# Kernel optimization log

Hardware: AMD Instinct MI355X
Metric: run time of the kernel (lower is better)

## Reference

```python
import jax, jax.numpy as jnp
import numpy as np

ID, IH, IW = 8, 16, 16
HEADS, DIM_HEAD = 8, 32
INP, OUP = 256, 256
B = 4
N = ID * IH * IW  # 2048
INNER = HEADS * DIM_HEAD  # 256
SCALE = DIM_HEAD ** -0.5


def _make_relative_pos():
    # Faithful to the torch ctor: 3D coords, pairwise diffs, linearize, shift to >=0
    z, y, x = np.meshgrid(np.arange(ID), np.arange(IH), np.arange(IW), indexing='ij')
    coords = np.stack([z.ravel(), y.ravel(), x.ravel()], axis=1)  # [N,3]
    rel = coords[:, None, :] - coords[None, :, :]                 # [N,N,3]
    rp = rel[:, :, 0] * (IH * IW) + rel[:, :, 1] * IW + rel[:, :, 2]
    rp = rp - rp.min()
    return jnp.asarray(rp, dtype=jnp.int32)                       # [N,N]


def setup_inputs() -> dict:
    key = jax.random.key(0)
    k1, k2, k3, k4, k5 = jax.random.split(key, 5)
    table_size = ID * IH * IW * 8  # 16384, as in nn.Embedding ctor
    return {
        "x": jax.random.normal(k1, (B, N, INP), dtype=jnp.float32),
        "w_qkv": jax.random.normal(k2, (INP, 3 * INNER), dtype=jnp.float32) * (INP ** -0.5),
        "bias_table": jax.random.normal(k3, (table_size, 1), dtype=jnp.float32),
        "w_out": jax.random.normal(k4, (INNER, OUP), dtype=jnp.float32) * (INNER ** -0.5),
        "b_out": jax.random.normal(k5, (OUP,), dtype=jnp.float32),
        "relative_pos": _make_relative_pos(),
    }


def reference(x, w_qkv, bias_table, w_out, b_out, relative_pos):
    Bb, Nn, C = x.shape
    qkv = x @ w_qkv                                   # [B, N, 3*H*D]
    qkv = qkv.reshape(Bb, Nn, 3, HEADS, DIM_HEAD)
    qkv = jnp.transpose(qkv, (2, 0, 3, 1, 4))         # [3, B, H, N, D]
    q, k, v = qkv[0], qkv[1], qkv[2]
    q = q * SCALE
    attn = jnp.einsum('bhnd,bhmd->bhnm', q, k)        # [B, H, N, N]
    bias = bias_table[relative_pos, 0]                # [N, N], shared across B,H
    attn = attn + bias
    attn = jax.nn.softmax(attn, axis=-1)
    out = jnp.einsum('bhnm,bhmd->bhnd', attn, v)      # [B, H, N, D]
    out = jnp.transpose(out, (0, 2, 1, 3)).reshape(Bb, Nn, INNER)
    return out @ w_out + b_out                        # dropout p=0 -> identity
```

## Files before the change

kernel.cpp:

```cpp
#include <hip/hip_runtime.h>

typedef unsigned short u16;
typedef unsigned int u32;
typedef __attribute__((ext_vector_type(8))) short bf16x8;
typedef __attribute__((ext_vector_type(4))) float f32x4;

#define MFMA16(a, b, c) __builtin_amdgcn_mfma_f32_16x16x32_bf16(a, b, c, 0, 0, 0)

__device__ __forceinline__ float hw_exp2(float x) { return __builtin_amdgcn_exp2f(x); }

__device__ __forceinline__ u16 f2bf(float f) {
    union { float f; u32 i; } v; v.f = f;
    u32 x = v.i;
    return (u16)((x + 0x7FFFu + ((x >> 16) & 1u)) >> 16);
}

__global__ __launch_bounds__(256) void k_prep(const float* __restrict__ x,
                                              const float* __restrict__ wqkv,
                                              const float* __restrict__ wout,
                                              u16* __restrict__ xb,
                                              u16* __restrict__ wqkvT,
                                              u16* __restrict__ woutT) {
    const float QSCALE2 = 0.2550566756538019f;
    int bx = blockIdx.x, tid = threadIdx.x;
    if (bx < 1024) {
        int base = bx * 2048 + tid * 8;
        float4 a = *(const float4*)(x + base);
        float4 b = *(const float4*)(x + base + 4);
        uint4 r;
        r.x = f2bf(a.x) | ((u32)f2bf(a.y) << 16);
        r.y = f2bf(a.z) | ((u32)f2bf(a.w) << 16);
        r.z = f2bf(b.x) | ((u32)f2bf(b.y) << 16);
        r.w = f2bf(b.z) | ((u32)f2bf(b.w) << 16);
        *(uint4*)(xb + base) = r;
    } else if (bx < 1792) {
        int idx = (bx - 1024) * 256 + tid;
        int n = idx >> 8, kk = idx & 255;
        float sc = (n < 256) ? QSCALE2 : 1.0f;
        wqkvT[idx] = f2bf(wqkv[kk * 768 + n] * sc);
    } else {
        int idx = (bx - 1792) * 256 + tid;
        int n = idx >> 8, kk = idx & 255;
        woutT[idx] = f2bf(wout[kk * 256 + n]);
    }
}

__global__ __launch_bounds__(256) void k_gemm_qkv(const u16* __restrict__ xb,
                                                  const u16* __restrict__ wT,
                                                  u16* __restrict__ qkv) {
    __shared__ __align__(16) u16 slds[8704];
    const int tid = threadIdx.x;
    const int wave = tid >> 6, lane = tid & 63, quad = lane >> 4, ql = lane & 15;
    const int mbase = blockIdx.x * 128 + (wave & 1) * 64;
    const int nbase = blockIdx.y * 64 + (wave >> 1) * 32;
    f32x4 acc[4][2];
#pragma unroll
    for (int i = 0; i < 4; ++i)
#pragma unroll
        for (int j = 0; j < 2; ++j) acc[i][j] = (f32x4){0.f, 0.f, 0.f, 0.f};
#pragma unroll
    for (int ks = 0; ks < 8; ++ks) {
        bf16x8 af[4], bfm[2];
#pragma unroll
        for (int ms = 0; ms < 4; ++ms)
            af[ms] = *(const bf16x8*)(xb + (size_t)(mbase + ms * 16 + ql) * 256 + ks * 32 + quad * 8);
#pragma unroll
        for (int ns = 0; ns < 2; ++ns)
            bfm[ns] = *(const bf16x8*)(wT + (size_t)(nbase + ns * 16 + ql) * 256 + ks * 32 + quad * 8);
#pragma unroll
        for (int ms = 0; ms < 4; ++ms)
#pragma unroll
            for (int ns = 0; ns < 2; ++ns)
                acc[ms][ns] = MFMA16(af[ms], bfm[ns], acc[ms][ns]);
    }

    const int t = (blockIdx.y * 64) >> 8;
    if (t < 2) {
        const int rowb = (wave & 1) * 64, colb = (wave >> 1) * 32;
#pragma unroll
        for (int ms = 0; ms < 4; ++ms)
#pragma unroll
            for (int ns = 0; ns < 2; ++ns)
#pragma unroll
                for (int r = 0; r < 4; ++r)
                    slds[(rowb + ms * 16 + quad * 4 + r) * 68 + colb + ns * 16 + ql] =
                        f2bf(acc[ms][ns][r]);
        __syncthreads();
        u16* base = qkv + (size_t)t * 2097152;
#pragma unroll
        for (int p = 0; p < 8; ++p) {
            int c = p * 256 + tid;
            int row = c >> 4, ch = c & 15;
            uint2 w = *(const uint2*)&slds[row * 68 + ch * 4];
            int n = blockIdx.x * 128 + row;
            int col = blockIdx.y * 64 + ch * 4;
            int h = (col & 255) >> 5, d = col & 31;
            *(uint2*)(base + ((size_t)((n >> 11) * 8 + h) * 2048 + (n & 2047)) * 32 + d) = w;
        }
    } else {
        const int hl = wave >> 1, nb = (wave & 1) * 64;
#pragma unroll
        for (int ms = 0; ms < 4; ++ms)
#pragma unroll
            for (int ns = 0; ns < 2; ++ns) {
                u16 e0 = f2bf(acc[ms][ns][0]), e1 = f2bf(acc[ms][ns][1]);
                u16 e2 = f2bf(acc[ms][ns][2]), e3 = f2bf(acc[ms][ns][3]);
                uint2 pp; pp.x = e0 | ((u32)e1 << 16); pp.y = e2 | ((u32)e3 << 16);
                *(uint2*)&slds[(hl * 32 + ns * 16 + ql) * 136 + nb + ms * 16 + quad * 4] = pp;
            }
        __syncthreads();
        u16* vbase = qkv + (size_t)2 * 2097152;
#pragma unroll
        for (int p = 0; p < 4; ++p) {
            int c = p * 256 + tid;
            int row = c >> 4, ch = c & 15;
            bf16x8 w = *(const bf16x8*)&slds[row * 136 + ch * 8];
            int n0 = blockIdx.x * 128 + ch * 8;
            int h = (blockIdx.y & 3) * 2 + (row >> 5), d = row & 31;
            *(bf16x8*)(vbase + (size_t)((n0 >> 11) * 8 + h) * 65536 +
                       (size_t)d * 2048 + (n0 & 2047)) = w;
        }
    }
}

__global__ __launch_bounds__(256, 4) void k_attn(const u16* __restrict__ q,
                                                 const u16* __restrict__ k,
                                                 const u16* __restrict__ vT,
                                                 const float* __restrict__ table,
                                                 u16* __restrict__ att) {
    __shared__ __align__(16) u16 kbuf[2][2][2048];
    __shared__ __align__(16) u16 vbuf[2][2][2048];
    __shared__ float tbl2[2176];
    __shared__ u32 pT[8][16 * 36];
    const int tid = threadIdx.x;
    const int bh = blockIdx.x & 31, qt = blockIdx.x >> 5;
    const int wave = tid >> 6, lane = tid & 63, quad = lane >> 4, ql = lane & 15;
    const float LOG2E = 1.4426950408889634f;

    const u16* kbh = k + (size_t)bh * 65536;
    const u16* vbh = vT + (size_t)bh * 65536;

    const int krow = wave * 16 + (lane >> 2);
    const u16* kg = kbh + krow * 32 + ((((lane & 3) ^ ((lane >> 3) & 3))) << 3);
    const int vd = wave * 8 + (lane >> 3);
    const u16* vg = vbh + (size_t)vd * 2048 + (((lane & 7) ^ (vd & 7)) << 3);

#define GLDS(SRC, DST) __builtin_amdgcn_global_load_lds(                         \
        (const __attribute__((address_space(1))) void*)(SRC),                    \
        (__attribute__((address_space(3))) void*)(DST), 16, 0, 0)
#define DMA(BUF, PAIR) do {                                                      \
    GLDS(kg + (PAIR) * 4096,        &kbuf[BUF][0][wave * 512]);                  \
    GLDS(kg + (PAIR) * 4096 + 2048, &kbuf[BUF][1][wave * 512]);                  \
    GLDS(vg + (PAIR) * 128,         &vbuf[BUF][0][wave * 512]);                  \
    GLDS(vg + (PAIR) * 128 + 64,    &vbuf[BUF][1][wave * 512]);                  \
} while (0)

    DMA(0, 0);

    const float4* tg = (const float4*)(table + qt * 128);
    for (int i = tid; i < 544; i += 256) {
        float4 t = tg[i];
        t.x *= LOG2E; t.y *= LOG2E; t.z *= LOG2E; t.w *= LOG2E;
        ((float4*)tbl2)[i] = t;
    }

    const int qr0 = qt * 128 + wave * 32 + ql;
    bf16x8 qf[2];
    qf[0] = *(const bf16x8*)(q + ((size_t)bh * 2048 + qr0) * 32 + quad * 8);
    qf[1] = *(const bf16x8*)(q + ((size_t)bh * 2048 + qr0 + 16) * 32 + quad * 8);
    const int bloc0 = wave * 32 + ql + 2047 - quad * 4;
    const int kro = ((quad ^ ((ql >> 1) & 3)) << 3);
    const int pbase = ql * 36;

    bf16x8 ones;
#pragma unroll
    for (int i = 0; i < 8; ++i) ones[i] = (short)0x3F80;

    f32x4 oT0[2], oT1[2], oL[2];
#pragma unroll
    for (int qh = 0; qh < 2; ++qh) {
        oT0[qh] = (f32x4){0.f, 0.f, 0.f, 0.f};
        oT1[qh] = (f32x4){0.f, 0.f, 0.f, 0.f};
        oL[qh]  = (f32x4){0.f, 0.f, 0.f, 0.f};
    }

    __syncthreads();

    for (int pr = 0; pr < 16; ++pr) {
        const int buf = pr & 1;
        if (pr < 15) DMA(buf ^ 1, pr + 1);

#pragma unroll
        for (int t = 0; t < 2; ++t) {
            const int kt = pr * 2 + t;
            const u16* kb = &kbuf[buf][t][0];
            const u16* vb = &vbuf[buf][t][0];
            bf16x8 kf[4], vf[4];
#pragma unroll
            for (int j = 0; j < 4; ++j)
                kf[j] = *(const bf16x8*)(kb + (j * 16 + ql) * 32 + kro);
#pragma unroll
            for (int f = 0; f < 4; ++f) {
                int c = f >> 1, dt = f & 1;
                vf[f] = *(const bf16x8*)(vb + (dt * 16 + ql) * 64 +
                                         (((c * 4 + quad) ^ (ql & 7)) << 3));
            }

#pragma unroll
            for (int qh = 0; qh < 2; ++qh) {
                f32x4 z = {0.f, 0.f, 0.f, 0.f};
                f32x4 s[4];
#pragma unroll
                for (int j = 0; j < 4; ++j) s[j] = MFMA16(kf[j], qf[qh], z);
#pragma unroll
                for (int j = 0; j < 4; ++j) {
                    const float* tb = &tbl2[bloc0 + qh * 16 - kt * 64 - j * 16 - 3];
#pragma unroll
                    for (int r = 0; r < 4; ++r)
                        s[j][r] = hw_exp2(s[j][r] + tb[3 - r]);
                }
                u32* pw = &pT[wave * 2 + qh][0];
#pragma unroll
                for (int j = 0; j < 4; ++j) {
                    uint2 w;
                    w.x = __builtin_amdgcn_perm(__float_as_uint(s[j][1]),
                                                __float_as_uint(s[j][0]), 0x07060302u);
                    w.y = __builtin_amdgcn_perm(__float_as_uint(s[j][3]),
                                                __float_as_uint(s[j][2]), 0x07060302u);
                    *(uint2*)&pw[pbase + j * 8 + quad * 2] = w;
                }
#pragma unroll
                for (int c = 0; c < 2; ++c) {
                    bf16x8 pa = *(const bf16x8*)&pw[pbase + c * 16 + quad * 4];
                    oT0[qh] = MFMA16(vf[c * 2 + 0], pa, oT0[qh]);
                    oT1[qh] = MFMA16(vf[c * 2 + 1], pa, oT1[qh]);
                    oL[qh]  = MFMA16(ones, pa, oL[qh]);
                }
            }
        }
        __syncthreads();
    }
#undef DMA
#undef GLDS

#pragma unroll
    for (int qh = 0; qh < 2; ++qh) {
        float inv = 1.0f / oL[qh][0];
        size_t base = ((size_t)bh * 2048 + qr0 + qh * 16) * 32;
#pragma unroll
        for (int dt = 0; dt < 2; ++dt) {
            const f32x4& o = dt ? oT1[qh] : oT0[qh];
            u16 e0 = f2bf(o[0] * inv), e1 = f2bf(o[1] * inv);
            u16 e2 = f2bf(o[2] * inv), e3 = f2bf(o[3] * inv);
            uint2 pp; pp.x = e0 | ((u32)e1 << 16); pp.y = e2 | ((u32)e3 << 16);
            *(uint2*)(att + base + dt * 16 + quad * 4) = pp;
        }
    }
}

__global__ __launch_bounds__(256) void k_gemm_out(const u16* __restrict__ attq,
                                                  const u16* __restrict__ wT,
                                                  const float* __restrict__ bout,
                                                  float* __restrict__ out) {
    const int tid = threadIdx.x;
    const int wave = tid >> 6, lane = tid & 63, quad = lane >> 4, ql = lane & 15;
    const int mbase = blockIdx.x * 128 + (wave & 1) * 64;
    const int nbase = blockIdx.y * 64 + (wave >> 1) * 32;
    f32x4 acc[4][2];
#pragma unroll
    for (int i = 0; i < 4; ++i)
#pragma unroll
        for (int j = 0; j < 2; ++j) acc[i][j] = (f32x4){0.f, 0.f, 0.f, 0.f};
#pragma unroll
    for (int ks = 0; ks < 8; ++ks) {
        bf16x8 af[4], bfm[2];
#pragma unroll
        for (int ms = 0; ms < 4; ++ms) {
            int row = mbase + ms * 16 + ql;
            af[ms] = *(const bf16x8*)(attq +
                ((size_t)((row >> 11) * 8 + ks) * 2048 + (row & 2047)) * 32 + quad * 8);
        }
#pragma unroll
        for (int ns = 0; ns < 2; ++ns)
            bfm[ns] = *(const bf16x8*)(wT + (size_t)(nbase + ns * 16 + ql) * 256 + ks * 32 + quad * 8);
#pragma unroll
        for (int ms = 0; ms < 4; ++ms)
#pragma unroll
            for (int ns = 0; ns < 2; ++ns)
                acc[ms][ns] = MFMA16(af[ms], bfm[ns], acc[ms][ns]);
    }
#pragma unroll
    for (int ms = 0; ms < 4; ++ms)
#pragma unroll
        for (int ns = 0; ns < 2; ++ns)
#pragma unroll
            for (int r = 0; r < 4; ++r) {
                int Mrow = mbase + ms * 16 + quad * 4 + r;
                int col = nbase + ns * 16 + ql;
                out[(size_t)Mrow * 256 + col] = acc[ms][ns][r] + bout[col];
            }
}

extern "C" void kernel_launch(void* const* d_in, const int* in_sizes, int n_in,
                              void* d_out, int out_size, void* d_ws, size_t ws_size,
                              hipStream_t stream) {
    const float* x    = (const float*)d_in[0];
    const float* wqkv = (const float*)d_in[1];
    const float* btab = (const float*)d_in[2];
    const float* wout = (const float*)d_in[3];
    const float* bout = (const float*)d_in[4];
    float* out = (float*)d_out;

    if (ws_size < (size_t)13107200) return;
    u16* ws = (u16*)d_ws;
    u16* wqkvT = ws;
    u16* woutT = wqkvT + 196608;
    u16* qkv   = woutT + 65536;
    u16* xb    = (u16*)d_out;

    hipLaunchKernelGGL(k_prep, dim3(2048), dim3(256), 0, stream, x, wqkv, wout, xb, wqkvT, woutT);
    hipLaunchKernelGGL(k_gemm_qkv, dim3(64, 12), dim3(256), 0, stream, xb, wqkvT, qkv);
    hipLaunchKernelGGL(k_attn, dim3(512), dim3(256), 0, stream,
                       qkv, qkv + 2097152, qkv + 2 * 2097152, btab, qkv);
    hipLaunchKernelGGL(k_gemm_out, dim3(64, 4), dim3(256), 0, stream, qkv, woutT, bout, out);
}
```

Before: 146.5 us.

## Load K/V fragments directly from global into registers with software double-buffering

```diff
diff --git a/kernel.cpp b/kernel.cpp
--- a/kernel.cpp
+++ b/kernel.cpp
@@ -128,8 +128,6 @@
                                                  const u16* __restrict__ vT,
                                                  const float* __restrict__ table,
                                                  u16* __restrict__ att) {
-    __shared__ __align__(16) u16 kbuf[2][2][2048];
-    __shared__ __align__(16) u16 vbuf[2][2][2048];
     __shared__ float tbl2[2176];
     __shared__ u32 pT[8][16 * 36];
     const int tid = threadIdx.x;
@@ -140,36 +138,19 @@
     const u16* kbh = k + (size_t)bh * 65536;
     const u16* vbh = vT + (size_t)bh * 65536;
 
-    const int krow = wave * 16 + (lane >> 2);
-    const u16* kg = kbh + krow * 32 + ((((lane & 3) ^ ((lane >> 3) & 3))) << 3);
-    const int vd = wave * 8 + (lane >> 3);
-    const u16* vg = vbh + (size_t)vd * 2048 + (((lane & 7) ^ (vd & 7)) << 3);
-
-#define GLDS(SRC, DST) __builtin_amdgcn_global_load_lds(                         \
-        (const __attribute__((address_space(1))) void*)(SRC),                    \
-        (__attribute__((address_space(3))) void*)(DST), 16, 0, 0)
-#define DMA(BUF, PAIR) do {                                                      \
-    GLDS(kg + (PAIR) * 4096,        &kbuf[BUF][0][wave * 512]);                  \
-    GLDS(kg + (PAIR) * 4096 + 2048, &kbuf[BUF][1][wave * 512]);                  \
-    GLDS(vg + (PAIR) * 128,         &vbuf[BUF][0][wave * 512]);                  \
-    GLDS(vg + (PAIR) * 128 + 64,    &vbuf[BUF][1][wave * 512]);                  \
-} while (0)
-
-    DMA(0, 0);
-
     const float4* tg = (const float4*)(table + qt * 128);
     for (int i = tid; i < 544; i += 256) {
         float4 t = tg[i];
         t.x *= LOG2E; t.y *= LOG2E; t.z *= LOG2E; t.w *= LOG2E;
         ((float4*)tbl2)[i] = t;
     }
+    __syncthreads();
 
     const int qr0 = qt * 128 + wave * 32 + ql;
     bf16x8 qf[2];
     qf[0] = *(const bf16x8*)(q + ((size_t)bh * 2048 + qr0) * 32 + quad * 8);
     qf[1] = *(const bf16x8*)(q + ((size_t)bh * 2048 + qr0 + 16) * 32 + quad * 8);
     const int bloc0 = wave * 32 + ql + 2047 - quad * 4;
-    const int kro = ((quad ^ ((ql >> 1) & 3)) << 3);
     const int pbase = ql * 36;
 
     bf16x8 ones;
@@ -184,64 +165,60 @@
         oL[qh]  = (f32x4){0.f, 0.f, 0.f, 0.f};
     }
 
-    __syncthreads();
-
-    for (int pr = 0; pr < 16; ++pr) {
-        const int buf = pr & 1;
-        if (pr < 15) DMA(buf ^ 1, pr + 1);
-
-#pragma unroll
-        for (int t = 0; t < 2; ++t) {
-            const int kt = pr * 2 + t;
-            const u16* kb = &kbuf[buf][t][0];
-            const u16* vb = &vbuf[buf][t][0];
-            bf16x8 kf[4], vf[4];
-#pragma unroll
-            for (int j = 0; j < 4; ++j)
-                kf[j] = *(const bf16x8*)(kb + (j * 16 + ql) * 32 + kro);
-#pragma unroll
-            for (int f = 0; f < 4; ++f) {
-                int c = f >> 1, dt = f & 1;
-                vf[f] = *(const bf16x8*)(vb + (dt * 16 + ql) * 64 +
-                                         (((c * 4 + quad) ^ (ql & 7)) << 3));
-            }
-
-#pragma unroll
-            for (int qh = 0; qh < 2; ++qh) {
-                f32x4 z = {0.f, 0.f, 0.f, 0.f};
-                f32x4 s[4];
-#pragma unroll
-                for (int j = 0; j < 4; ++j) s[j] = MFMA16(kf[j], qf[qh], z);
-#pragma unroll
-                for (int j = 0; j < 4; ++j) {
-                    const float* tb = &tbl2[bloc0 + qh * 16 - kt * 64 - j * 16 - 3];
-#pragma unroll
-                    for (int r = 0; r < 4; ++r)
-                        s[j][r] = hw_exp2(s[j][r] + tb[3 - r]);
-                }
-                u32* pw = &pT[wave * 2 + qh][0];
-#pragma unroll
-                for (int j = 0; j < 4; ++j) {
-                    uint2 w;
-                    w.x = __builtin_amdgcn_perm(__float_as_uint(s[j][1]),
-                                                __float_as_uint(s[j][0]), 0x07060302u);
-                    w.y = __builtin_amdgcn_perm(__float_as_uint(s[j][3]),
-                                                __float_as_uint(s[j][2]), 0x07060302u);
-                    *(uint2*)&pw[pbase + j * 8 + quad * 2] = w;
-                }
-#pragma unroll
-                for (int c = 0; c < 2; ++c) {
-                    bf16x8 pa = *(const bf16x8*)&pw[pbase + c * 16 + quad * 4];
-                    oT0[qh] = MFMA16(vf[c * 2 + 0], pa, oT0[qh]);
-                    oT1[qh] = MFMA16(vf[c * 2 + 1], pa, oT1[qh]);
-                    oL[qh]  = MFMA16(ones, pa, oL[qh]);
-                }
-            }
-        }
-        __syncthreads();
-    }
-#undef DMA
-#undef GLDS
+#define LOADG(KF, VF, KT) do {                                                          \
+    _Pragma("unroll") for (int j_ = 0; j_ < 4; ++j_)                                    \
+        KF[j_] = *(const bf16x8*)(kbh + (size_t)((KT) * 64 + j_ * 16 + ql) * 32 + quad * 8); \
+    _Pragma("unroll") for (int f_ = 0; f_ < 4; ++f_) {                                  \
+        int c_ = f_ >> 1, dt_ = f_ & 1;                                                 \
+        VF[f_] = *(const bf16x8*)(vbh + (size_t)(dt_ * 16 + ql) * 2048 +                \
+                                  (KT) * 64 + c_ * 32 + quad * 8); }                    \
+} while (0)
+
+#define BODY(KF, VF, KT) do {                                                           \
+    _Pragma("unroll") for (int qh_ = 0; qh_ < 2; ++qh_) {                               \
+        f32x4 z_ = {0.f, 0.f, 0.f, 0.f};                                                \
+        f32x4 s_[4];                                                                    \
+        _Pragma("unroll") for (int j_ = 0; j_ < 4; ++j_)                                \
+            s_[j_] = MFMA16(KF[j_], qf[qh_], z_);                                       \
+        _Pragma("unroll") for (int j_ = 0; j_ < 4; ++j_) {                              \
+            const float* tb_ = &tbl2[bloc0 + qh_ * 16 - (KT) * 64 - j_ * 16 - 3];       \
+            _Pragma("unroll") for (int r_ = 0; r_ < 4; ++r_)                            \
+                s_[j_][r_] = hw_exp2(s_[j_][r_] + tb_[3 - r_]);                         \
+        }                                                                               \
+        u32* pw_ = &pT[wave * 2 + qh_][0];                                              \
+        _Pragma("unroll") for (int j_ = 0; j_ < 4; ++j_) {                              \
+            uint2 w_;                                                                   \
+            w_.x = __builtin_amdgcn_perm(__float_as_uint(s_[j_][1]),                    \
+                                         __float_as_uint(s_[j_][0]), 0x07060302u);      \
+            w_.y = __builtin_amdgcn_perm(__float_as_uint(s_[j_][3]),                    \
+                                         __float_as_uint(s_[j_][2]), 0x07060302u);      \
+            *(uint2*)&pw_[pbase + j_ * 8 + quad * 2] = w_;                              \
+        }                                                                               \
+        _Pragma("unroll") for (int c_ = 0; c_ < 2; ++c_) {                              \
+            bf16x8 pa_ = *(const bf16x8*)&pw_[pbase + c_ * 16 + quad * 4];              \
+            oT0[qh_] = MFMA16(VF[c_ * 2 + 0], pa_, oT0[qh_]);                           \
+            oT1[qh_] = MFMA16(VF[c_ * 2 + 1], pa_, oT1[qh_]);                           \
+            oL[qh_]  = MFMA16(ones, pa_, oL[qh_]);                                      \
+        }                                                                               \
+    }                                                                                   \
+} while (0)
+
+    bf16x8 kfA[4], vfA[4], kfB[4], vfB[4];
+    LOADG(kfA, vfA, 0);
+    __builtin_amdgcn_sched_barrier(0);
+    for (int kt2 = 0; kt2 < 16; ++kt2) {
+        LOADG(kfB, vfB, 2 * kt2 + 1);
+        __builtin_amdgcn_sched_barrier(0);
+        BODY(kfA, vfA, 2 * kt2);
+        __builtin_amdgcn_sched_barrier(0);
+        int ktC = (kt2 == 15) ? 31 : (2 * kt2 + 2);
+        LOADG(kfA, vfA, ktC);
+        __builtin_amdgcn_sched_barrier(0);
+        BODY(kfB, vfB, 2 * kt2 + 1);
+        __builtin_amdgcn_sched_barrier(0);
+    }
+#undef LOADG
+#undef BODY
 
 #pragma unroll
     for (int qh = 0; qh < 2; ++qh) {
```

After: 230.0 us. 1.57x slower.

## Feed softmax probabilities to PV MFMA directly from registers via 16x16x16 MFMA

Applied to the files above, without the earlier changes.

```diff
diff --git a/kernel.cpp b/kernel.cpp
--- a/kernel.cpp
+++ b/kernel.cpp
@@ -3,9 +3,11 @@
 typedef unsigned short u16;
 typedef unsigned int u32;
 typedef __attribute__((ext_vector_type(8))) short bf16x8;
+typedef __attribute__((ext_vector_type(4))) short bf16x4;
 typedef __attribute__((ext_vector_type(4))) float f32x4;
 
 #define MFMA16(a, b, c) __builtin_amdgcn_mfma_f32_16x16x32_bf16(a, b, c, 0, 0, 0)
+#define MFMAK16(a, b, c) __builtin_amdgcn_mfma_f32_16x16x16bf16_1k(a, b, c, 0, 0, 0)
 
 __device__ __forceinline__ float hw_exp2(float x) { return __builtin_amdgcn_exp2f(x); }
 
@@ -123,7 +125,7 @@
     }
 }
 
-__global__ __launch_bounds__(256, 4) void k_attn(const u16* __restrict__ q,
+__global__ __launch_bounds__(256, 2) void k_attn(const u16* __restrict__ q,
                                                  const u16* __restrict__ k,
                                                  const u16* __restrict__ vT,
                                                  const float* __restrict__ table,
@@ -131,7 +133,6 @@
     __shared__ __align__(16) u16 kbuf[2][2][2048];
     __shared__ __align__(16) u16 vbuf[2][2][2048];
     __shared__ float tbl2[2176];
-    __shared__ u32 pT[8][16 * 36];
     const int tid = threadIdx.x;
     const int bh = blockIdx.x & 31, qt = blockIdx.x >> 5;
     const int wave = tid >> 6, lane = tid & 63, quad = lane >> 4, ql = lane & 15;
@@ -170,11 +171,10 @@
     qf[1] = *(const bf16x8*)(q + ((size_t)bh * 2048 + qr0 + 16) * 32 + quad * 8);
     const int bloc0 = wave * 32 + ql + 2047 - quad * 4;
     const int kro = ((quad ^ ((ql >> 1) & 3)) << 3);
-    const int pbase = ql * 36;
-
-    bf16x8 ones;
-#pragma unroll
-    for (int i = 0; i < 8; ++i) ones[i] = (short)0x3F80;
+
+    bf16x4 ones4;
+#pragma unroll
+    for (int i = 0; i < 4; ++i) ones4[i] = (short)0x3F80;
 
     f32x4 oT0[2], oT1[2], oL[2];
 #pragma unroll
@@ -195,16 +195,27 @@
             const int kt = pr * 2 + t;
             const u16* kb = &kbuf[buf][t][0];
             const u16* vb = &vbuf[buf][t][0];
-            bf16x8 kf[4], vf[4];
+            bf16x8 kf[4];
+            bf16x4 va[2][4];
 #pragma unroll
             for (int j = 0; j < 4; ++j)
                 kf[j] = *(const bf16x8*)(kb + (j * 16 + ql) * 32 + kro);
 #pragma unroll
-            for (int f = 0; f < 4; ++f) {
-                int c = f >> 1, dt = f & 1;
-                vf[f] = *(const bf16x8*)(vb + (dt * 16 + ql) * 64 +
-                                         (((c * 4 + quad) ^ (ql & 7)) << 3));
-            }
+            for (int dt = 0; dt < 2; ++dt)
+#pragma unroll
+                for (int j = 0; j < 4; ++j) {
+                    int nloc = j * 16 + quad * 4;
+                    int slot = (nloc >> 3) ^ (ql & 7);
+                    va[dt][j] = *(const bf16x4*)(vb + (dt * 16 + ql) * 64 +
+                                                 slot * 8 + (nloc & 7));
+                }
+            const int bkt = bloc0 - kt * 64;
+            float bg[5][4];
+#pragma unroll
+            for (int g = 0; g < 5; ++g)
+#pragma unroll
+                for (int r = 0; r < 4; ++r)
+                    bg[g][r] = tbl2[bkt + 16 * g - 48 - r];
 
 #pragma unroll
             for (int qh = 0; qh < 2; ++qh) {
@@ -213,28 +224,20 @@
 #pragma unroll
                 for (int j = 0; j < 4; ++j) s[j] = MFMA16(kf[j], qf[qh], z);
 #pragma unroll
+                for (int j = 0; j < 4; ++j)
+#pragma unroll
+                    for (int r = 0; r < 4; ++r)
+                        s[j][r] = hw_exp2(s[j][r] + bg[qh + 3 - j][r]);
+#pragma unroll
                 for (int j = 0; j < 4; ++j) {
-                    const float* tb = &tbl2[bloc0 + qh * 16 - kt * 64 - j * 16 - 3];
-#pragma unroll
-                    for (int r = 0; r < 4; ++r)
-                        s[j][r] = hw_exp2(s[j][r] + tb[3 - r]);
-                }
-                u32* pw = &pT[wave * 2 + qh][0];
-#pragma unroll
-                for (int j = 0; j < 4; ++j) {
-                    uint2 w;
-                    w.x = __builtin_amdgcn_perm(__float_as_uint(s[j][1]),
-                                                __float_as_uint(s[j][0]), 0x07060302u);
-                    w.y = __builtin_amdgcn_perm(__float_as_uint(s[j][3]),
-                                                __float_as_uint(s[j][2]), 0x07060302u);
-                    *(uint2*)&pw[pbase + j * 8 + quad * 2] = w;
-                }
-#pragma unroll
-                for (int c = 0; c < 2; ++c) {
-                    bf16x8 pa = *(const bf16x8*)&pw[pbase + c * 16 + quad * 4];
-                    oT0[qh] = MFMA16(vf[c * 2 + 0], pa, oT0[qh]);
-                    oT1[qh] = MFMA16(vf[c * 2 + 1], pa, oT1[qh]);
-                    oL[qh]  = MFMA16(ones, pa, oL[qh]);
+                    union { u32 u[2]; bf16x4 v; } pj;
+                    pj.u[0] = __builtin_amdgcn_perm(__float_as_uint(s[j][1]),
+                                                    __float_as_uint(s[j][0]), 0x07060302u);
+                    pj.u[1] = __builtin_amdgcn_perm(__float_as_uint(s[j][3]),
+                                                    __float_as_uint(s[j][2]), 0x07060302u);
+                    oT0[qh] = MFMAK16(va[0][j], pj.v, oT0[qh]);
+                    oT1[qh] = MFMAK16(va[1][j], pj.v, oT1[qh]);
+                    oL[qh]  = MFMAK16(ones4, pj.v, oL[qh]);
                 }
             }
         }
```

Result: faster. 141.6 us, median of 3 (-3.4%).
